# Performance work log

Hardware: AMD Instinct MI355X
Metric: run time of the kernel (lower is better)

## Reference

```python
import jax, jax.numpy as jnp
import numpy as np

NEG_INF = float(np.finfo(np.float32).min)
CHUNK = 8          # chunk_size
EPS = 1e-6         # eps
SHARP = 1.0        # sharpening_factor
B, KLEN, KDIM, QDIM, ADIM, VDIM = 16, 4096, 512, 512, 512, 512


def moving_sum(x, back, forward):
    # x: [B, T]; moving_sum[i] = sum_{j=i-back}^{i+forward} x[j] (zero-padded)
    T = x.shape[1]
    cs = jnp.cumsum(jnp.pad(x, ((0, 0), (back + 1, forward))), axis=1)
    return cs[:, back + forward + 1:] - cs[:, :T]


def energy(key, query, Wk, bk, Wq, vw, mask_bk, r):
    # key: [B,K,kdim], query: [B,1,qdim], vw: [adim]
    kp = jnp.einsum('bkd,da->bka', key, Wk) + bk
    qp = jnp.einsum('bqd,da->bqa', query, Wq)
    e = jnp.einsum('bka,a->bk', jax.nn.relu(kp + qp), vw)
    if r is not None:
        e = e + r
    return jnp.where(mask_bk, e, NEG_INF)


def setup_inputs() -> dict:
    key = jax.random.key(0)
    ks = jax.random.split(key, 12)
    inp = {
        'key': jax.random.normal(ks[0], (B, KLEN, KDIM), jnp.float32),
        'value': jax.random.normal(ks[1], (B, KLEN, VDIM), jnp.float32),
        'query': jax.random.normal(ks[2], (B, 1, QDIM), jnp.float32),
        'mask': jnp.ones((B, 1, KLEN), bool),
        'aw_prev': jnp.zeros((B, KLEN, 1), jnp.float32).at[:, 0, 0].set(1.0),
        'noise': jax.random.normal(ks[3], (B, KLEN), jnp.float32),  # noise_std=1.0
        # monotonic Energy params (v is weight-normed: w = g * v/||v||, plus offset r)
        'Wk_m': jax.random.normal(ks[4], (KDIM, ADIM), jnp.float32) * 0.02,
        'bk_m': jnp.zeros((ADIM,), jnp.float32),
        'Wq_m': jax.random.normal(ks[5], (QDIM, ADIM), jnp.float32) * 0.02,
        'v_m': jax.random.normal(ks[6], (ADIM,), jnp.float32),
        'g_m': jnp.asarray(np.sqrt(1.0 / ADIM), jnp.float32),
        'r_m': jnp.asarray(-4.0, jnp.float32),
        # chunk Energy params (plain v, no r)
        'Wk_c': jax.random.normal(ks[7], (KDIM, ADIM), jnp.float32) * 0.02,
        'bk_c': jnp.zeros((ADIM,), jnp.float32),
        'Wq_c': jax.random.normal(ks[8], (QDIM, ADIM), jnp.float32) * 0.02,
        'v_c': jax.random.normal(ks[9], (ADIM,), jnp.float32) * 0.02,
    }
    return inp


def reference(key, value, query, mask, aw_prev, noise,
              Wk_m, bk_m, Wq_m, v_m, g_m, r_m,
              Wk_c, bk_c, Wq_c, v_c):
    mask_bk = mask[:, 0, :]  # [B, K], qmax == 1
    # --- monotonic attention (mode='parallel') ---
    vw_m = g_m * v_m / jnp.linalg.norm(v_m)
    e_mono = energy(key, query, Wk_m, bk_m, Wq_m, vw_m, mask_bk, r_m)
    p_choose = jax.nn.sigmoid(e_mono + noise)  # gaussian-noised sigmoid
    # safe_cumprod: exp(exclusive cumsum of log(clamp(1-p, eps, 1)))
    log1mp = jnp.log(jnp.clip(1.0 - p_choose, EPS, 1.0))
    cumprod_1mp = jnp.exp(jnp.cumsum(jnp.pad(log1mp[:, :-1], ((0, 0), (1, 0))), axis=1))
    alpha = p_choose * cumprod_1mp * jnp.cumsum(
        aw_prev[:, :, 0] / jnp.clip(cumprod_1mp, EPS, 1.0), axis=1)
    # --- chunkwise attention beta ---
    e_chunk = energy(key, query, Wk_c, bk_c, Wq_c, v_c, mask_bk, None)
    e_chunk = e_chunk - jnp.max(e_chunk, axis=1, keepdims=True)
    softmax_exp = jnp.maximum(jnp.exp(e_chunk), 1e-5)
    denom = moving_sum(softmax_exp, CHUNK - 1, 0)
    beta = softmax_exp * moving_sum(alpha * SHARP / denom, 0, CHUNK - 1)
    # context vector over values with beta (chunk_size > 1 path)
    cv = jnp.einsum('bk,bkd->bd', beta, value)[:, None, :]  # [B,1,value_dim]
    return cv, alpha[:, :, None], beta
```

## Files before the change

### kernel.cpp

```cpp
#include <hip/hip_runtime.h>
#include <hip/hip_bf16.h>
#include <math.h>

#define NB    16
#define KLEN  4096
#define KDIM  512
#define ADIM  512
#define NCOMB 1024
#define EPSF  1e-6f

typedef __bf16 bf16x8 __attribute__((ext_vector_type(8)));
typedef float  f32x4  __attribute__((ext_vector_type(4)));
typedef unsigned short ushort4v __attribute__((ext_vector_type(4)));

static __device__ __forceinline__ unsigned short f2bf(float f) {
  union { __hip_bfloat16 h; unsigned short u; } v;
  v.h = __float2bfloat16(f);
  return v.u;
}

__global__ void zero_two(float* __restrict__ e_ws, float* __restrict__ cv) {
  int i = blockIdx.x * 256 + threadIdx.x;
  if (i < 2 * NB * KLEN) e_ws[i] = 0.f;
  else {
    int j = i - 2 * NB * KLEN;
    if (j < NB * 512) cv[j] = 0.f;
  }
}

__global__ __launch_bounds__(512) void prep_vw(const float* __restrict__ v_m,
                                               const float* __restrict__ g_ptr,
                                               const float* __restrict__ v_c,
                                               float* __restrict__ vw_comb) {
  __shared__ float red[512];
  int t = threadIdx.x;
  float x = v_m[t];
  red[t] = x * x;
  __syncthreads();
  for (int off = 256; off > 0; off >>= 1) {
    if (t < off) red[t] += red[t + off];
    __syncthreads();
  }
  float inv = g_ptr[0] / sqrtf(red[0]);
  vw_comb[t] = x * inv;
  vw_comb[512 + t] = v_c[t];
}

__global__ __launch_bounds__(256) void prep_q(const float* __restrict__ query,
                                              const float* __restrict__ Wq_m,
                                              const float* __restrict__ bk_m,
                                              const float* __restrict__ Wq_c,
                                              const float* __restrict__ bk_c,
                                              float* __restrict__ q_comb) {
  int b = blockIdx.x, t = threadIdx.x;
  __shared__ float q[512];
  q[t] = query[b * 512 + t];
  q[t + 256] = query[b * 512 + 256 + t];
  __syncthreads();
  float am0 = 0.f, am1 = 0.f, ac0 = 0.f, ac1 = 0.f;
  for (int d = 0; d < 512; ++d) {
    float qd = q[d];
    am0 += qd * Wq_m[d * 512 + t];
    am1 += qd * Wq_m[d * 512 + 256 + t];
    ac0 += qd * Wq_c[d * 512 + t];
    ac1 += qd * Wq_c[d * 512 + 256 + t];
  }
  q_comb[b * 1024 + t]       = am0 + bk_m[t];
  q_comb[b * 1024 + 256 + t] = am1 + bk_m[256 + t];
  q_comb[b * 1024 + 512 + t] = ac0 + bk_c[t];
  q_comb[b * 1024 + 768 + t] = ac1 + bk_c[256 + t];
}

__global__ __launch_bounds__(256) void prep_wt(const float* __restrict__ Wk_m,
                                               const float* __restrict__ Wk_c,
                                               unsigned short* __restrict__ WT) {
  int i = blockIdx.x * 256 + threadIdx.x;
  int a = i >> 9, d = i & 511;
  float v = (a < 512) ? Wk_m[d * 512 + a] : Wk_c[d * 512 + (a - 512)];
  WT[i] = f2bf(v);
}

#define BM 128
#define BN 128
#define BK 32

__global__ __launch_bounds__(256) void energy_gemm(
    const float* __restrict__ key,
    const unsigned short* __restrict__ WT,
    const float* __restrict__ q_comb,
    const float* __restrict__ vw_comb,
    float* __restrict__ e_mono,
    float* __restrict__ e_chunk) {
  __shared__ unsigned short As[2][BM][BK];
  __shared__ unsigned short Bs[2][BN][BK];

  int tid = threadIdx.x;
  int lane = tid & 63;
  int wid = tid >> 6;
  int wm = wid >> 1, wn = wid & 1;
  long rowBase = (long)blockIdx.x * BM;
  int ncolBase = blockIdx.y * BN;
  int b = (int)(rowBase >> 12);

  f32x4 acc[4][4] = {};

  int arow = tid >> 3;
  int ak   = (tid & 7) * 4;

  auto stage = [&](int buf, int k0) {
    #pragma unroll
    for (int i = 0; i < 4; ++i) {
      int r = arow + i * 32;
      f32x4 kv = *reinterpret_cast<const f32x4*>(&key[(rowBase + r) * KDIM + (k0 + ak)]);
      ushort4v pk = { f2bf(kv[0]), f2bf(kv[1]), f2bf(kv[2]), f2bf(kv[3]) };
      *reinterpret_cast<ushort4v*>(&As[buf][r][ak]) = pk;
      ushort4v wv = *reinterpret_cast<const ushort4v*>(&WT[(long)(ncolBase + r) * KDIM + (k0 + ak)]);
      *reinterpret_cast<ushort4v*>(&Bs[buf][r][ak]) = wv;
    }
  };

  stage(0, 0);
  __syncthreads();

  const int nsteps = KDIM / BK;
  int lrow = lane & 15;
  int lk = (lane >> 4) * 8;
  for (int s = 0; s < nsteps; ++s) {
    int buf = s & 1;
    if (s + 1 < nsteps) stage(buf ^ 1, (s + 1) * BK);
    bf16x8 af[4], bfr[4];
    #pragma unroll
    for (int m = 0; m < 4; ++m)
      af[m] = *reinterpret_cast<const bf16x8*>(&As[buf][wm * 64 + m * 16 + lrow][lk]);
    #pragma unroll
    for (int n = 0; n < 4; ++n)
      bfr[n] = *reinterpret_cast<const bf16x8*>(&Bs[buf][wn * 64 + n * 16 + lrow][lk]);
    #pragma unroll
    for (int m = 0; m < 4; ++m)
      #pragma unroll
      for (int n = 0; n < 4; ++n)
        acc[m][n] = __builtin_amdgcn_mfma_f32_16x16x32_bf16(af[m], bfr[n], acc[m][n], 0, 0, 0);
    __syncthreads();
  }

  float qv[4], vv[4];
  #pragma unroll
  for (int n = 0; n < 4; ++n) {
    int ncol = ncolBase + wn * 64 + n * 16 + lrow;
    qv[n] = q_comb[b * 1024 + ncol];
    vv[n] = vw_comb[ncol];
  }
  float* e_out = (blockIdx.y < 4) ? e_mono : e_chunk;
  int rowInB = (int)(rowBase & (KLEN - 1));
  #pragma unroll
  for (int m = 0; m < 4; ++m) {
    #pragma unroll
    for (int j = 0; j < 4; ++j) {
      float s_ = 0.f;
      #pragma unroll
      for (int n = 0; n < 4; ++n) {
        float v = acc[m][n][j] + qv[n];
        v = v > 0.f ? v : 0.f;
        s_ += v * vv[n];
      }
      s_ += __shfl_xor(s_, 1);
      s_ += __shfl_xor(s_, 2);
      s_ += __shfl_xor(s_, 4);
      s_ += __shfl_xor(s_, 8);
      if ((lane & 15) == 0) {
        int row = rowInB + wm * 64 + m * 16 + ((lane >> 4) * 4 + j);
        atomicAdd(&e_out[b * KLEN + row], s_);
      }
    }
  }
}

__global__ __launch_bounds__(1024) void scan_kernel(
    const float* __restrict__ e_mono, const float* __restrict__ e_chunk,
    const float* __restrict__ noise, const float* __restrict__ aw_prev,
    const float* __restrict__ r_ptr,
    float* __restrict__ out_alpha, float* __restrict__ out_beta) {
  __shared__ float sh_a[4096];
  __shared__ float sh_s[4096];
  __shared__ float sh_t[4096];
  __shared__ float red[1024];

  int b = blockIdx.x, t = threadIdx.x;
  int base = b * KLEN + t * 4;
  float r = r_ptr[0];

  f32x4 em = *(const f32x4*)&e_mono[base];
  f32x4 nz = *(const f32x4*)&noise[base];
  float pch[4], lp[4], pre1[4];
  float tot1 = 0.f;
  #pragma unroll
  for (int j = 0; j < 4; ++j) {
    float x = em[j] + r + nz[j];
    float p = 1.f / (1.f + expf(-x));
    float omp = fminf(fmaxf(1.f - p, EPSF), 1.f);
    pch[j] = p;
    pre1[j] = tot1;
    lp[j] = logf(omp);
    tot1 += lp[j];
  }
  red[t] = tot1; __syncthreads();
  float v1 = tot1;
  for (int off = 1; off < 1024; off <<= 1) {
    float add = (t >= off) ? red[t - off] : 0.f;
    __syncthreads();
    v1 += add;
    red[t] = v1;
    __syncthreads();
  }
  float excl1 = v1 - tot1;

  f32x4 aw = *(const f32x4*)&aw_prev[base];
  float cp[4], uu[4], pre2[4];
  float tot2 = 0.f;
  #pragma unroll
  for (int j = 0; j < 4; ++j) {
    cp[j] = expf(excl1 + pre1[j]);
    float cpc = fminf(fmaxf(cp[j], EPSF), 1.f);
    uu[j] = aw[j] / cpc;
    pre2[j] = tot2;
    tot2 += uu[j];
  }
  __syncthreads();
  red[t] = tot2; __syncthreads();
  float v2 = tot2;
  for (int off = 1; off < 1024; off <<= 1) {
    float add = (t >= off) ? red[t - off] : 0.f;
    __syncthreads();
    v2 += add;
    red[t] = v2;
    __syncthreads();
  }
  float excl2 = v2 - tot2;
  #pragma unroll
  for (int j = 0; j < 4; ++j) {
    float al = pch[j] * cp[j] * (excl2 + pre2[j] + uu[j]);
    sh_a[t * 4 + j] = al;
    out_alpha[base + j] = al;
  }

  f32x4 ec = *(const f32x4*)&e_chunk[base];
  float mx = fmaxf(fmaxf(ec[0], ec[1]), fmaxf(ec[2], ec[3]));
  __syncthreads();
  red[t] = mx; __syncthreads();
  for (int off = 512; off > 0; off >>= 1) {
    if (t < off) red[t] = fmaxf(red[t], red[t + off]);
    __syncthreads();
  }
  float bmax = red[0];
  #pragma unroll
  for (int j = 0; j < 4; ++j)
    sh_s[t * 4 + j] = fmaxf(expf(ec[j] - bmax), 1e-5f);
  __syncthreads();
  #pragma unroll
  for (int j = 0; j < 4; ++j) {
    int k = t * 4 + j;
    float d = 0.f;
    int lo = k - 7 < 0 ? 0 : k - 7;
    for (int q = lo; q <= k; ++q) d += sh_s[q];
    sh_t[k] = sh_a[k] / d;
  }
  __syncthreads();
  #pragma unroll
  for (int j = 0; j < 4; ++j) {
    int k = t * 4 + j;
    int hi = k + 7 > KLEN - 1 ? KLEN - 1 : k + 7;
    float s = 0.f;
    for (int q = k; q <= hi; ++q) s += sh_t[q];
    out_beta[base + j] = sh_s[k] * s;
  }
}

__global__ __launch_bounds__(256) void cv_kernel(const float* __restrict__ beta,
                                                 const float* __restrict__ value,
                                                 float* __restrict__ cv) {
  int b = blockIdx.x >> 5;
  int kc = blockIdx.x & 31;
  int t = threadIdx.x;
  __shared__ float bsh[128];
  int k0 = kc * 128;
  if (t < 128) bsh[t] = beta[b * KLEN + k0 + t];
  __syncthreads();
  float a0 = 0.f, a1 = 0.f;
  const float* vp = &value[((long)b * KLEN + k0) * 512];
  for (int k = 0; k < 128; ++k) {
    a0 += bsh[k] * vp[(long)k * 512 + t];
    a1 += bsh[k] * vp[(long)k * 512 + 256 + t];
  }
  atomicAdd(&cv[b * 512 + t], a0);
  atomicAdd(&cv[b * 512 + t + 256], a1);
}

extern "C" void kernel_launch(void* const* d_in, const int* in_sizes, int n_in,
                              void* d_out, int out_size, void* d_ws, size_t ws_size,
                              hipStream_t stream) {
  const float* key     = (const float*)d_in[0];
  const float* value   = (const float*)d_in[1];
  const float* query   = (const float*)d_in[2];
  const float* aw_prev = (const float*)d_in[4];
  const float* noise   = (const float*)d_in[5];
  const float* Wk_m    = (const float*)d_in[6];
  const float* bk_m    = (const float*)d_in[7];
  const float* Wq_m    = (const float*)d_in[8];
  const float* v_m     = (const float*)d_in[9];
  const float* g_m     = (const float*)d_in[10];
  const float* r_m     = (const float*)d_in[11];
  const float* Wk_c    = (const float*)d_in[12];
  const float* bk_c    = (const float*)d_in[13];
  const float* Wq_c    = (const float*)d_in[14];
  const float* v_c     = (const float*)d_in[15];

  float* out_cv    = (float*)d_out;
  float* out_alpha = (float*)d_out + NB * 512;
  float* out_beta  = out_alpha + NB * KLEN;

  float* e_mono  = (float*)d_ws;
  float* e_chunk = e_mono + NB * KLEN;
  float* q_comb  = e_chunk + NB * KLEN;
  float* vw_comb = q_comb + NB * 1024;
  unsigned short* WT = (unsigned short*)(vw_comb + 1024);

  hipLaunchKernelGGL(zero_two, dim3((2 * NB * KLEN + NB * 512 + 255) / 256), dim3(256), 0, stream,
                     e_mono, out_cv);
  hipLaunchKernelGGL(prep_vw, dim3(1), dim3(512), 0, stream, v_m, g_m, v_c, vw_comb);
  hipLaunchKernelGGL(prep_q, dim3(NB), dim3(256), 0, stream, query, Wq_m, bk_m, Wq_c, bk_c, q_comb);
  hipLaunchKernelGGL(prep_wt, dim3(NCOMB * KDIM / 256), dim3(256), 0, stream, Wk_m, Wk_c, WT);
  hipLaunchKernelGGL(energy_gemm, dim3((NB * KLEN) / BM, NCOMB / BN), dim3(256), 0, stream,
                     key, WT, q_comb, vw_comb, e_mono, e_chunk);
  hipLaunchKernelGGL(scan_kernel, dim3(NB), dim3(1024), 0, stream,
                     e_mono, e_chunk, noise, aw_prev, r_m, out_alpha, out_beta);
  hipLaunchKernelGGL(cv_kernel, dim3(NB * 32), dim3(256), 0, stream,
                     out_beta, value, out_cv);
}
```

Before: 500.0 us.

## Keep full key row-tile resident in LDS and stream pre-tiled weights

The energy GEMM now loads a 128-row key tile entirely into LDS once, converted to bf16 with an XOR swizzle. It then streams all 1024 output columns of pre-tiled bf16 weights through a double buffer using global_load_lds, accumulating the ReLU-dot in LDS and writing e_mono/e_chunk directly, without global atomics or a zeroing pass. This removes the 8x re-read and re-conversion of key across column blocks. The scan kernel swaps its LDS Hillis-Steele scans and reductions for wave shuffles plus a per-wave prefix, and prep_q is split over 8 d-chunks with atomics for more parallelism. The cost is heavy LDS use (about 145KB per block) that limits occupancy, plus 128 serial sync steps per block.

```diff
diff --git a/kernel.cpp b/kernel.cpp
--- a/kernel.cpp
+++ b/kernel.cpp
@@ -5,13 +5,12 @@
 #define NB    16
 #define KLEN  4096
 #define KDIM  512
-#define ADIM  512
-#define NCOMB 1024
 #define EPSF  1e-6f
 
 typedef __bf16 bf16x8 __attribute__((ext_vector_type(8)));
 typedef float  f32x4  __attribute__((ext_vector_type(4)));
 typedef unsigned short ushort4v __attribute__((ext_vector_type(4)));
+typedef unsigned short ushort8v __attribute__((ext_vector_type(8)));
 
 static __device__ __forceinline__ unsigned short f2bf(float f) {
   union { __hip_bfloat16 h; unsigned short u; } v;
@@ -19,13 +18,17 @@
   return v.u;
 }
 
-__global__ void zero_two(float* __restrict__ e_ws, float* __restrict__ cv) {
+static __device__ __forceinline__ void gload_lds16(const void* g, void* l) {
+  __builtin_amdgcn_global_load_lds(
+      (const __attribute__((address_space(1))) unsigned int*)g,
+      (__attribute__((address_space(3))) unsigned int*)l, 16, 0, 0);
+}
+
+__global__ void zero_ws(float* __restrict__ cv, float* __restrict__ q_comb) {
   int i = blockIdx.x * 256 + threadIdx.x;
-  if (i < 2 * NB * KLEN) e_ws[i] = 0.f;
-  else {
-    int j = i - 2 * NB * KLEN;
-    if (j < NB * 512) cv[j] = 0.f;
-  }
+  if (i < NB * 512) cv[i] = 0.f;
+  int j = i - NB * 512;
+  if (j >= 0 && j < NB * 1024) q_comb[j] = 0.f;
 }
 
 __global__ __launch_bounds__(512) void prep_vw(const float* __restrict__ v_m,
@@ -52,125 +55,148 @@
                                               const float* __restrict__ Wq_c,
                                               const float* __restrict__ bk_c,
                                               float* __restrict__ q_comb) {
-  int b = blockIdx.x, t = threadIdx.x;
-  __shared__ float q[512];
-  q[t] = query[b * 512 + t];
-  q[t + 256] = query[b * 512 + 256 + t];
+  __shared__ float qsh[64];
+  int b = blockIdx.x, dc = blockIdx.y, t = threadIdx.x;
+  if (t < 64) qsh[t] = query[b * 512 + dc * 64 + t];
   __syncthreads();
   float am0 = 0.f, am1 = 0.f, ac0 = 0.f, ac1 = 0.f;
-  for (int d = 0; d < 512; ++d) {
-    float qd = q[d];
+  for (int i = 0; i < 64; ++i) {
+    float qd = qsh[i];
+    int d = dc * 64 + i;
     am0 += qd * Wq_m[d * 512 + t];
     am1 += qd * Wq_m[d * 512 + 256 + t];
     ac0 += qd * Wq_c[d * 512 + t];
     ac1 += qd * Wq_c[d * 512 + 256 + t];
   }
-  q_comb[b * 1024 + t]       = am0 + bk_m[t];
-  q_comb[b * 1024 + 256 + t] = am1 + bk_m[256 + t];
-  q_comb[b * 1024 + 512 + t] = ac0 + bk_c[t];
-  q_comb[b * 1024 + 768 + t] = ac1 + bk_c[256 + t];
+  if (dc == 0) {
+    am0 += bk_m[t];  am1 += bk_m[256 + t];
+    ac0 += bk_c[t];  ac1 += bk_c[256 + t];
+  }
+  atomicAdd(&q_comb[b * 1024 + t],       am0);
+  atomicAdd(&q_comb[b * 1024 + 256 + t], am1);
+  atomicAdd(&q_comb[b * 1024 + 512 + t], ac0);
+  atomicAdd(&q_comb[b * 1024 + 768 + t], ac1);
 }
 
 __global__ __launch_bounds__(256) void prep_wt(const float* __restrict__ Wk_m,
                                                const float* __restrict__ Wk_c,
-                                               unsigned short* __restrict__ WT) {
-  int i = blockIdx.x * 256 + threadIdx.x;
-  int a = i >> 9, d = i & 511;
-  float v = (a < 512) ? Wk_m[d * 512 + a] : Wk_c[d * 512 + (a - 512)];
-  WT[i] = f2bf(v);
-}
-
-#define BM 128
-#define BN 128
-#define BK 32
-
-__global__ __launch_bounds__(256) void energy_gemm(
+                                               unsigned short* __restrict__ WT_pre) {
+  int tile = blockIdx.x;
+  int nt = tile >> 4, s = tile & 15;
+  int t = threadIdx.x;
+  int n = t >> 1, k0 = (t & 1) * 16;
+  int acol = nt * 128 + n;
+  const float* W = (acol < 512) ? Wk_m : Wk_c;
+  int col = acol & 511;
+  ushort8v o0, o1;
+  #pragma unroll
+  for (int i = 0; i < 8; ++i)
+    o0[i] = f2bf(W[(s * 32 + k0 + i) * 512 + col]);
+  #pragma unroll
+  for (int i = 0; i < 8; ++i)
+    o1[i] = f2bf(W[(s * 32 + k0 + 8 + i) * 512 + col]);
+  size_t base = (size_t)tile * 4096 + (size_t)t * 16;
+  *reinterpret_cast<ushort8v*>(&WT_pre[base])     = o0;
+  *reinterpret_cast<ushort8v*>(&WT_pre[base + 8]) = o1;
+}
+
+__global__ __launch_bounds__(512, 2) void energy_gemm(
     const float* __restrict__ key,
-    const unsigned short* __restrict__ WT,
+    const unsigned short* __restrict__ WT_pre,
     const float* __restrict__ q_comb,
     const float* __restrict__ vw_comb,
     float* __restrict__ e_mono,
     float* __restrict__ e_chunk) {
-  __shared__ unsigned short As[2][BM][BK];
-  __shared__ unsigned short Bs[2][BN][BK];
+  __shared__ unsigned short As[128 * 512];
+  __shared__ unsigned short Bs[2][4096];
+  __shared__ float e_acc[128][4];
 
   int tid = threadIdx.x;
   int lane = tid & 63;
   int wid = tid >> 6;
-  int wm = wid >> 1, wn = wid & 1;
-  long rowBase = (long)blockIdx.x * BM;
-  int ncolBase = blockIdx.y * BN;
+  int wm = wid >> 2;
+  int wn = wid & 3;
+  long rowBase = (long)blockIdx.x * 128;
   int b = (int)(rowBase >> 12);
 
-  f32x4 acc[4][4] = {};
-
-  int arow = tid >> 3;
-  int ak   = (tid & 7) * 4;
-
-  auto stage = [&](int buf, int k0) {
+  ((float*)e_acc)[tid] = 0.f;
+
+  gload_lds16((const char*)WT_pre + (size_t)tid * 16,
+              (char*)(&Bs[0][0]) + wid * 1024);
+
+  #pragma unroll
+  for (int i = 0; i < 32; ++i) {
+    int idx4 = i * 512 + tid;
+    int row = idx4 >> 7;
+    int col4 = idx4 & 127;
+    f32x4 kv = *reinterpret_cast<const f32x4*>(&key[(rowBase + row) * KDIM + col4 * 4]);
+    ushort4v pk = { f2bf(kv[0]), f2bf(kv[1]), f2bf(kv[2]), f2bf(kv[3]) };
+    int byte = row * 1024 + ((col4 * 8) ^ ((row & 7) << 4));
+    *reinterpret_cast<ushort4v*>((char*)As + byte) = pk;
+  }
+  __syncthreads();
+
+  int lrow = lane & 15;
+  int kh = lane >> 4;
+  f32x4 acc[4][2] = {};
+
+  for (int nt = 0; nt < 8; ++nt) {
+    for (int s = 0; s < 16; ++s) {
+      int tt = nt * 16 + s;
+      if (tt + 1 < 128)
+        gload_lds16((const char*)WT_pre + (size_t)(tt + 1) * 8192 + (size_t)tid * 16,
+                    (char*)(&Bs[(tt + 1) & 1][0]) + wid * 1024);
+      const char* Bbase = (const char*)(&Bs[tt & 1][0]);
+      bf16x8 af[4], bfr[2];
+      #pragma unroll
+      for (int m = 0; m < 4; ++m) {
+        int rowa = wm * 64 + m * 16 + lrow;
+        int byte = rowa * 1024 + ((s * 64 + kh * 16) ^ ((rowa & 7) << 4));
+        af[m] = *reinterpret_cast<const bf16x8*>((const char*)As + byte);
+      }
+      #pragma unroll
+      for (int nf = 0; nf < 2; ++nf) {
+        int rowb = wn * 32 + nf * 16 + lrow;
+        bfr[nf] = *reinterpret_cast<const bf16x8*>(Bbase + rowb * 64 + kh * 16);
+      }
+      #pragma unroll
+      for (int m = 0; m < 4; ++m)
+        #pragma unroll
+        for (int nf = 0; nf < 2; ++nf)
+          acc[m][nf] = __builtin_amdgcn_mfma_f32_16x16x32_bf16(af[m], bfr[nf], acc[m][nf], 0, 0, 0);
+      __syncthreads();
+    }
+    int col0 = nt * 128 + wn * 32 + lrow;
+    float q0 = q_comb[b * 1024 + col0];
+    float q1 = q_comb[b * 1024 + col0 + 16];
+    float w0 = vw_comb[col0];
+    float w1 = vw_comb[col0 + 16];
     #pragma unroll
-    for (int i = 0; i < 4; ++i) {
-      int r = arow + i * 32;
-      f32x4 kv = *reinterpret_cast<const f32x4*>(&key[(rowBase + r) * KDIM + (k0 + ak)]);
-      ushort4v pk = { f2bf(kv[0]), f2bf(kv[1]), f2bf(kv[2]), f2bf(kv[3]) };
-      *reinterpret_cast<ushort4v*>(&As[buf][r][ak]) = pk;
-      ushort4v wv = *reinterpret_cast<const ushort4v*>(&WT[(long)(ncolBase + r) * KDIM + (k0 + ak)]);
-      *reinterpret_cast<ushort4v*>(&Bs[buf][r][ak]) = wv;
+    for (int m = 0; m < 4; ++m) {
+      #pragma unroll
+      for (int j = 0; j < 4; ++j) {
+        float v0 = acc[m][0][j] + q0; v0 = v0 > 0.f ? v0 : 0.f;
+        float v1 = acc[m][1][j] + q1; v1 = v1 > 0.f ? v1 : 0.f;
+        float sv = v0 * w0 + v1 * w1;
+        sv += __shfl_xor(sv, 1);
+        sv += __shfl_xor(sv, 2);
+        sv += __shfl_xor(sv, 4);
+        sv += __shfl_xor(sv, 8);
+        if (lrow == 0)
+          e_acc[wm * 64 + m * 16 + kh * 4 + j][wn] += sv;
+      }
+      acc[m][0] = (f32x4){0.f, 0.f, 0.f, 0.f};
+      acc[m][1] = (f32x4){0.f, 0.f, 0.f, 0.f};
     }
-  };
-
-  stage(0, 0);
-  __syncthreads();
-
-  const int nsteps = KDIM / BK;
-  int lrow = lane & 15;
-  int lk = (lane >> 4) * 8;
-  for (int s = 0; s < nsteps; ++s) {
-    int buf = s & 1;
-    if (s + 1 < nsteps) stage(buf ^ 1, (s + 1) * BK);
-    bf16x8 af[4], bfr[4];
-    #pragma unroll
-    for (int m = 0; m < 4; ++m)
-      af[m] = *reinterpret_cast<const bf16x8*>(&As[buf][wm * 64 + m * 16 + lrow][lk]);
-    #pragma unroll
-    for (int n = 0; n < 4; ++n)
-      bfr[n] = *reinterpret_cast<const bf16x8*>(&Bs[buf][wn * 64 + n * 16 + lrow][lk]);
-    #pragma unroll
-    for (int m = 0; m < 4; ++m)
-      #pragma unroll
-      for (int n = 0; n < 4; ++n)
-        acc[m][n] = __builtin_amdgcn_mfma_f32_16x16x32_bf16(af[m], bfr[n], acc[m][n], 0, 0, 0);
-    __syncthreads();
-  }
-
-  float qv[4], vv[4];
-  #pragma unroll
-  for (int n = 0; n < 4; ++n) {
-    int ncol = ncolBase + wn * 64 + n * 16 + lrow;
-    qv[n] = q_comb[b * 1024 + ncol];
-    vv[n] = vw_comb[ncol];
-  }
-  float* e_out = (blockIdx.y < 4) ? e_mono : e_chunk;
-  int rowInB = (int)(rowBase & (KLEN - 1));
-  #pragma unroll
-  for (int m = 0; m < 4; ++m) {
-    #pragma unroll
-    for (int j = 0; j < 4; ++j) {
-      float s_ = 0.f;
-      #pragma unroll
-      for (int n = 0; n < 4; ++n) {
-        float v = acc[m][n][j] + qv[n];
-        v = v > 0.f ? v : 0.f;
-        s_ += v * vv[n];
+    if (nt == 3 || nt == 7) {
+      __syncthreads();
+      if (tid < 128) {
+        float sum = e_acc[tid][0] + e_acc[tid][1] + e_acc[tid][2] + e_acc[tid][3];
+        e_acc[tid][0] = 0.f; e_acc[tid][1] = 0.f; e_acc[tid][2] = 0.f; e_acc[tid][3] = 0.f;
+        float* dst = (nt == 3) ? e_mono : e_chunk;
+        dst[rowBase + tid] = sum;
       }
-      s_ += __shfl_xor(s_, 1);
-      s_ += __shfl_xor(s_, 2);
-      s_ += __shfl_xor(s_, 4);
-      s_ += __shfl_xor(s_, 8);
-      if ((lane & 15) == 0) {
-        int row = rowInB + wm * 64 + m * 16 + ((lane >> 4) * 4 + j);
-        atomicAdd(&e_out[b * KLEN + row], s_);
-      }
+      __syncthreads();
     }
   }
 }
@@ -183,15 +209,16 @@
   __shared__ float sh_a[4096];
   __shared__ float sh_s[4096];
   __shared__ float sh_t[4096];
-  __shared__ float red[1024];
+  __shared__ float wred[16];
 
   int b = blockIdx.x, t = threadIdx.x;
+  int lane = t & 63, wid = t >> 6;
   int base = b * KLEN + t * 4;
   float r = r_ptr[0];
 
   f32x4 em = *(const f32x4*)&e_mono[base];
   f32x4 nz = *(const f32x4*)&noise[base];
-  float pch[4], lp[4], pre1[4];
+  float pch[4], pre1[4];
   float tot1 = 0.f;
   #pragma unroll
   for (int j = 0; j < 4; ++j) {
@@ -200,19 +227,20 @@
     float omp = fminf(fmaxf(1.f - p, EPSF), 1.f);
     pch[j] = p;
     pre1[j] = tot1;
-    lp[j] = logf(omp);
-    tot1 += lp[j];
-  }
-  red[t] = tot1; __syncthreads();
-  float v1 = tot1;
-  for (int off = 1; off < 1024; off <<= 1) {
-    float add = (t >= off) ? red[t - off] : 0.f;
-    __syncthreads();
-    v1 += add;
-    red[t] = v1;
-    __syncthreads();
-  }
-  float excl1 = v1 - tot1;
+    tot1 += logf(omp);
+  }
+  float v = tot1;
+  #pragma unroll
+  for (int off = 1; off < 64; off <<= 1) {
+    float u = __shfl_up(v, off);
+    if (lane >= off) v += u;
+  }
+  if (lane == 63) wred[wid] = v;
+  __syncthreads();
+  float pre = 0.f;
+  for (int w = 0; w < wid; ++w) pre += wred[w];
+  float excl1 = pre + (v - tot1);
+  __syncthreads();
 
   f32x4 aw = *(const f32x4*)&aw_prev[base];
   float cp[4], uu[4], pre2[4];
@@ -225,17 +253,17 @@
     pre2[j] = tot2;
     tot2 += uu[j];
   }
-  __syncthreads();
-  red[t] = tot2; __syncthreads();
-  float v2 = tot2;
-  for (int off = 1; off < 1024; off <<= 1) {
-    float add = (t >= off) ? red[t - off] : 0.f;
-    __syncthreads();
-    v2 += add;
-    red[t] = v2;
-    __syncthreads();
-  }
-  float excl2 = v2 - tot2;
+  v = tot2;
+  #pragma unroll
+  for (int off = 1; off < 64; off <<= 1) {
+    float u = __shfl_up(v, off);
+    if (lane >= off) v += u;
+  }
+  if (lane == 63) wred[wid] = v;
+  __syncthreads();
+  pre = 0.f;
+  for (int w = 0; w < wid; ++w) pre += wred[w];
+  float excl2 = pre + (v - tot2);
   #pragma unroll
   for (int j = 0; j < 4; ++j) {
     float al = pch[j] * cp[j] * (excl2 + pre2[j] + uu[j]);
@@ -245,13 +273,14 @@
 
   f32x4 ec = *(const f32x4*)&e_chunk[base];
   float mx = fmaxf(fmaxf(ec[0], ec[1]), fmaxf(ec[2], ec[3]));
-  __syncthreads();
-  red[t] = mx; __syncthreads();
-  for (int off = 512; off > 0; off >>= 1) {
-    if (t < off) red[t] = fmaxf(red[t], red[t + off]);
-    __syncthreads();
-  }
-  float bmax = red[0];
+  #pragma unroll
+  for (int off = 1; off < 64; off <<= 1)
+    mx = fmaxf(mx, __shfl_xor(mx, off));
+  __syncthreads();
+  if (lane == 0) wred[wid] = mx;
+  __syncthreads();
+  float bmax = wred[0];
+  for (int w = 1; w < 16; ++w) bmax = fmaxf(bmax, wred[w]);
   #pragma unroll
   for (int j = 0; j < 4; ++j)
     sh_s[t * 4 + j] = fmaxf(expf(ec[j] - bmax), 1e-5f);
@@ -259,8 +288,8 @@
   #pragma unroll
   for (int j = 0; j < 4; ++j) {
     int k = t * 4 + j;
+    int lo = k - 7 < 0 ? 0 : k - 7;
     float d = 0.f;
-    int lo = k - 7 < 0 ? 0 : k - 7;
     for (int q = lo; q <= k; ++q) d += sh_s[q];
     sh_t[k] = sh_a[k] / d;
   }
@@ -322,15 +351,15 @@
   float* e_chunk = e_mono + NB * KLEN;
   float* q_comb  = e_chunk + NB * KLEN;
   float* vw_comb = q_comb + NB * 1024;
-  unsigned short* WT = (unsigned short*)(vw_comb + 1024);
-
-  hipLaunchKernelGGL(zero_two, dim3((2 * NB * KLEN + NB * 512 + 255) / 256), dim3(256), 0, stream,
-                     e_mono, out_cv);
+  unsigned short* WT_pre = (unsigned short*)(vw_comb + 1024);
+
+  hipLaunchKernelGGL(zero_ws, dim3(96), dim3(256), 0, stream, out_cv, q_comb);
   hipLaunchKernelGGL(prep_vw, dim3(1), dim3(512), 0, stream, v_m, g_m, v_c, vw_comb);
-  hipLaunchKernelGGL(prep_q, dim3(NB), dim3(256), 0, stream, query, Wq_m, bk_m, Wq_c, bk_c, q_comb);
-  hipLaunchKernelGGL(prep_wt, dim3(NCOMB * KDIM / 256), dim3(256), 0, stream, Wk_m, Wk_c, WT);
-  hipLaunchKernelGGL(energy_gemm, dim3((NB * KLEN) / BM, NCOMB / BN), dim3(256), 0, stream,
-                     key, WT, q_comb, vw_comb, e_mono, e_chunk);
+  hipLaunchKernelGGL(prep_q, dim3(16, 8), dim3(256), 0, stream,
+                     query, Wq_m, bk_m, Wq_c, bk_c, q_comb);
+  hipLaunchKernelGGL(prep_wt, dim3(128), dim3(256), 0, stream, Wk_m, Wk_c, WT_pre);
+  hipLaunchKernelGGL(energy_gemm, dim3(512), dim3(512), 0, stream,
+                     key, WT_pre, q_comb, vw_comb, e_mono, e_chunk);
   hipLaunchKernelGGL(scan_kernel, dim3(NB), dim3(1024), 0, stream,
                      e_mono, e_chunk, noise, aw_prev, r_m, out_alpha, out_beta);
   hipLaunchKernelGGL(cv_kernel, dim3(NB * 32), dim3(256), 0, stream,
```

Measured after the change: 494.5 us. Within noise of the previous version (-1.1%).
